# Performance work log

Measured on AMD Instinct MI355X. Metric: run time of the kernel, lower is better.

Reference implementation:

```python
import jax, jax.numpy as jnp
import numpy as np

B, S, G, E = 2048, 32768, 4096, 1024  # batch, source_size, n_groups(target_size), embeddings_size


def setup_inputs() -> dict:
    key = jax.random.key(0)
    k_x, k_w, k_we, k_perm = jax.random.split(key, 4)
    x = jax.random.normal(k_x, (B, S), dtype=jnp.float32)
    W = jax.random.normal(k_w, (E, G), dtype=jnp.float32) * 0.02  # Linear(target_size -> embed, no bias)
    # per-element weights for 'w_sum' groups (concatenated Linear(group_size,1) weights)
    w_elem = jax.random.normal(k_we, (S,), dtype=jnp.float32) * 0.1
    perm = jax.random.permutation(k_perm, S).astype(jnp.int32)
    # ragged group boundaries: n_groups groups, each size >= 1, summing to S
    rng = np.random.default_rng(0)
    cuts = np.sort(rng.choice(np.arange(1, S), G - 1, replace=False))
    sizes = np.diff(np.concatenate([[0], cuts, [S]]))
    segment_ids = jnp.asarray(np.repeat(np.arange(G), sizes), dtype=jnp.int32)
    # aggregation type per group: 0='sum', 1='or', 2='w_sum'
    agg_type = jnp.asarray(rng.integers(0, 3, G), dtype=jnp.int32)
    return {"x": x, "W": W, "w_elem": w_elem, "perm": perm,
            "segment_ids": segment_ids, "agg_type": agg_type}


def reference(x, W, w_elem, perm, segment_ids, agg_type):
    # gather via groups_permute
    xp = x[:, perm]  # [B, S]
    # fused ragged per-group reductions, segment axis first: [S, B] -> [G, B]
    xt = xp.T
    seg_sum = jax.ops.segment_sum(xt, segment_ids, num_segments=G)              # jnp.sum per group
    seg_wsum = jax.ops.segment_sum(xt * w_elem[:, None], segment_ids, num_segments=G)  # Linear(g,1) per group
    seg_nnz = jax.ops.segment_sum((xt != 0).astype(x.dtype), segment_ids, num_segments=G)
    seg_or = (seg_nnz > 0).astype(x.dtype)                                       # jnp.any per group (bool -> float on hstack)
    a = agg_type[:, None]
    y = jnp.where(a == 0, seg_sum, jnp.where(a == 1, seg_or, seg_wsum)).T        # [B, G]
    # relu + Linear(target_size -> embeddings_size, no bias)
    return jnp.einsum('bg,eg->be', jax.nn.relu(y), W)
```

## Files before the change

kernel.cpp:

```cpp
#include <hip/hip_runtime.h>
#include <hip/hip_bf16.h>

#define B_DIM 2048
#define S_DIM 32768
#define G_DIM 4096
#define E_DIM 1024
#define KSPLIT 4
#define KCHUNK (G_DIM / KSPLIT)

typedef __bf16 bf16x8 __attribute__((ext_vector_type(8)));
typedef float f32x4 __attribute__((ext_vector_type(4)));

__device__ __forceinline__ unsigned short f2bf(float f) {
  unsigned int u = __builtin_bit_cast(unsigned int, f);
  u += 0x7FFFu + ((u >> 16) & 1u);
  return (unsigned short)(u >> 16);
}

__device__ __forceinline__ void async16(void* lds, const void* g) {
  __builtin_amdgcn_global_load_lds(
      (const __attribute__((address_space(1))) unsigned int*)g,
      (__attribute__((address_space(3))) unsigned int*)lds, 16, 0, 0);
}

__device__ __forceinline__ void lds_add(float* p, float v) {
  unsigned off = (unsigned)(size_t)(__attribute__((address_space(3))) float*)p;
  asm volatile("ds_add_f32 %0, %1" :: "v"(off), "v"(v));
}

__global__ __launch_bounds__(256) void setup_meta(
    const float* __restrict__ w_elem, const int* __restrict__ perm,
    const int* __restrict__ segid, const int* __restrict__ agg,
    unsigned* __restrict__ meta1) {
  int s = blockIdx.x * 256 + threadIdx.x;
  if (s >= S_DIM) return;
  int g = segid[s];
  int a = agg[g];
  float cm = (a == 0) ? 1.0f : (a == 2 ? w_elem[s] : 0.0f);
  meta1[s] = (unsigned)perm[s] | (a == 1 ? 0x8000u : 0u) |
             ((unsigned)f2bf(cm) << 16);
}

__global__ __launch_bounds__(256) void setup_runs(
    const int* __restrict__ segid, unsigned* __restrict__ metaH,
    unsigned short* __restrict__ metaG) {
  int t = blockIdx.x * 256 + threadIdx.x;
  if (t >= S_DIM / 32) return;
  int s0 = t * 32;
  int prev = (s0 == 0) ? -1 : segid[s0 - 1];
  unsigned m = 0;
#pragma unroll
  for (int c = 0; c < 8; ++c) {
    int4 gw = *reinterpret_cast<const int4*>(segid + s0 + c * 4);
    if (gw.x != prev) m |= 1u << (c * 4 + 0);
    if (gw.y != gw.x) m |= 1u << (c * 4 + 1);
    if (gw.z != gw.y) m |= 1u << (c * 4 + 2);
    if (gw.w != gw.z) m |= 1u << (c * 4 + 3);
    prev = gw.w;
  }
  metaH[t] = m;
  metaG[t] = (unsigned short)segid[s0];
}

__global__ __launch_bounds__(256) void conv_w(const float* __restrict__ W,
                                              unsigned short* __restrict__ Wb) {
  size_t i = ((size_t)blockIdx.x * 256 + threadIdx.x) * 4;
  float4 v = *reinterpret_cast<const float4*>(W + i);
  ushort4 o;
  o.x = f2bf(v.x);
  o.y = f2bf(v.y);
  o.z = f2bf(v.z);
  o.w = f2bf(v.w);
  *reinterpret_cast<ushort4*>(Wb + i) = o;
}

__global__ __launch_bounds__(1024, 8) void seg_reduce(
    const float* __restrict__ x, const unsigned* __restrict__ meta1,
    const unsigned* __restrict__ metaH, const unsigned short* __restrict__ metaG,
    const int* __restrict__ agg, unsigned short* __restrict__ y) {
  __shared__ unsigned short xrow[S_DIM];
  __shared__ float acc[G_DIM];
  const int t = threadIdx.x;
  const int b = blockIdx.x;

#pragma unroll
  for (int i = 0; i < G_DIM / 1024; ++i) acc[t + i * 1024] = 0.0f;

  const float4* xg = reinterpret_cast<const float4*>(x + (size_t)b * S_DIM);
#pragma unroll
  for (int i = 0; i < S_DIM / 4 / 1024; ++i) {
    float4 v = xg[i * 1024 + t];
    unsigned short h0 = __builtin_bit_cast(unsigned short, (__bf16)v.x);
    unsigned short h1 = __builtin_bit_cast(unsigned short, (__bf16)v.y);
    unsigned short h2 = __builtin_bit_cast(unsigned short, (__bf16)v.z);
    unsigned short h3 = __builtin_bit_cast(unsigned short, (__bf16)v.w);
    uint2 p;
    p.x = (unsigned)h0 | ((unsigned)h1 << 16);
    p.y = (unsigned)h2 | ((unsigned)h3 << 16);
    *reinterpret_cast<uint2*>(&xrow[(i * 1024 + t) * 4]) = p;
  }
  __syncthreads();

  const int s0 = t * 32;
  const unsigned mrun = metaH[t];
  const bool firstPlain = (mrun & 1u) != 0;
  int g = metaG[t];
  float sum = 0.0f;
  int nflush = 0;

  for (int h = 0; h < 2; ++h) {
    const int sb = s0 + h * 16;
    uint4 ma = *reinterpret_cast<const uint4*>(meta1 + sb);
    uint4 mb = *reinterpret_cast<const uint4*>(meta1 + sb + 4);
    uint4 mc = *reinterpret_cast<const uint4*>(meta1 + sb + 8);
    uint4 md = *reinterpret_cast<const uint4*>(meta1 + sb + 12);
    unsigned m[16] = {ma.x, ma.y, ma.z, ma.w, mb.x, mb.y, mb.z, mb.w,
                      mc.x, mc.y, mc.z, mc.w, md.x, md.y, md.z, md.w};
    unsigned short xu[16];
#pragma unroll
    for (int j = 0; j < 16; ++j) xu[j] = xrow[m[j] & 0x7FFF];
    const unsigned mh = mrun >> (h * 16);
#pragma unroll
    for (int j = 0; j < 16; ++j) {
      if (h + j > 0 && (mh & (1u << j))) {
        if (nflush == 0 && !firstPlain) {
          lds_add(&acc[g], sum);
        } else {
          acc[g] = sum;
        }
        ++nflush;
        sum = 0.0f;
        ++g;
      }
      float xv = __builtin_bit_cast(float, (unsigned)xu[j] << 16);
      float cm = __builtin_bit_cast(float, m[j] & 0xFFFF0000u);
      float v = (m[j] & 0x8000u) ? (xu[j] ? 1.0f : 0.0f) : xv * cm;
      sum += v;
    }
  }
  lds_add(&acc[g], sum);

  asm volatile("s_waitcnt lgkmcnt(0)" ::: "memory");
  __syncthreads();

#pragma unroll
  for (int i = 0; i < G_DIM / 1024; ++i) {
    int g2 = t + i * 1024;
    float v = acc[g2];
    if (agg[g2] == 1) v = (v > 0.0f) ? 1.0f : 0.0f;
    v = fmaxf(v, 0.0f);
    y[(size_t)b * G_DIM + g2] = f2bf(v);
  }
}

__global__ __launch_bounds__(256) void gemm_bt(
    const unsigned short* __restrict__ A,
    const unsigned short* __restrict__ Bw,
    float* __restrict__ part) {
  __shared__ __align__(16) unsigned short As[64 * 64];
  __shared__ __align__(16) unsigned short Bs[64 * 64];
  const int t = threadIdx.x;
  const int lane = t & 63;
  const int wid = t >> 6;
  const int wr = wid >> 1;
  const int wc = wid & 1;
  const int row0 = blockIdx.y * 64;
  const int col0 = blockIdx.x * 64;
  const int kc = blockIdx.z;

  const int r_ = t >> 3;
  const int s_ = t & 7;
  const int ksw = (s_ ^ (r_ & 7)) * 8;
  const unsigned short* Ag0 = A + (size_t)(row0 + r_) * G_DIM + ksw;
  const unsigned short* Ag1 = A + (size_t)(row0 + r_ + 32) * G_DIM + ksw;
  const unsigned short* Bg0 = Bw + (size_t)(col0 + r_) * G_DIM + ksw;
  const unsigned short* Bg1 = Bw + (size_t)(col0 + r_ + 32) * G_DIM + ksw;

  char* AsB = (char*)As;
  char* BsB = (char*)Bs;
  char* dA0 = AsB + wid * 1024;
  char* dA1 = AsB + 4096 + wid * 1024;
  char* dB0 = BsB + wid * 1024;
  char* dB1 = BsB + 4096 + wid * 1024;

  const int lm = lane & 15;
  const int lk = lane >> 4;

  f32x4 acc[2][2] = {};

  for (int kt = kc * KCHUNK; kt < (kc + 1) * KCHUNK; kt += 64) {
    async16(dA0, Ag0 + kt);
    async16(dA1, Ag1 + kt);
    async16(dB0, Bg0 + kt);
    async16(dB1, Bg1 + kt);
    __syncthreads();
#pragma unroll
    for (int kk = 0; kk < 2; ++kk) {
      bf16x8 af[2], bfr[2];
#pragma unroll
      for (int m = 0; m < 2; ++m) {
        int row = wr * 32 + m * 16 + lm;
        int slot = (kk * 4 + lk) ^ (row & 7);
        af[m] = *(const bf16x8*)(AsB + row * 128 + slot * 16);
      }
#pragma unroll
      for (int n = 0; n < 2; ++n) {
        int row = wc * 32 + n * 16 + lm;
        int slot = (kk * 4 + lk) ^ (row & 7);
        bfr[n] = *(const bf16x8*)(BsB + row * 128 + slot * 16);
      }
#pragma unroll
      for (int m = 0; m < 2; ++m)
#pragma unroll
        for (int n = 0; n < 2; ++n)
          acc[m][n] = __builtin_amdgcn_mfma_f32_16x16x32_bf16(af[m], bfr[n],
                                                              acc[m][n], 0, 0, 0);
    }
    __syncthreads();
  }

  float* P = part + (size_t)kc * B_DIM * E_DIM;
#pragma unroll
  for (int m = 0; m < 2; ++m) {
    int r = row0 + wr * 32 + m * 16 + lk * 4;
#pragma unroll
    for (int n = 0; n < 2; ++n) {
      int c = col0 + wc * 32 + n * 16 + lm;
#pragma unroll
      for (int q = 0; q < 4; ++q) {
        P[(size_t)(r + q) * E_DIM + c] = acc[m][n][q];
      }
    }
  }
}

__global__ __launch_bounds__(256) void reduce_part(
    const float* __restrict__ part, float* __restrict__ C) {
  const size_t i = ((size_t)blockIdx.x * 256 + threadIdx.x) * 4;
  const size_t n = (size_t)B_DIM * E_DIM;
  float4 v0 = *reinterpret_cast<const float4*>(part + i);
  float4 v1 = *reinterpret_cast<const float4*>(part + n + i);
  float4 v2 = *reinterpret_cast<const float4*>(part + 2 * n + i);
  float4 v3 = *reinterpret_cast<const float4*>(part + 3 * n + i);
  float4 o;
  o.x = (v0.x + v1.x) + (v2.x + v3.x);
  o.y = (v0.y + v1.y) + (v2.y + v3.y);
  o.z = (v0.z + v1.z) + (v2.z + v3.z);
  o.w = (v0.w + v1.w) + (v2.w + v3.w);
  *reinterpret_cast<float4*>(C + i) = o;
}

extern "C" void kernel_launch(void* const* d_in, const int* in_sizes, int n_in,
                              void* d_out, int out_size, void* d_ws, size_t ws_size,
                              hipStream_t stream) {
  const float* x = (const float*)d_in[0];
  const float* W = (const float*)d_in[1];
  const float* w_elem = (const float*)d_in[2];
  const int* perm = (const int*)d_in[3];
  const int* segid = (const int*)d_in[4];
  const int* agg = (const int*)d_in[5];
  float* out = (float*)d_out;

  char* ws = (char*)d_ws;
  unsigned short* y = (unsigned short*)ws;
  unsigned short* Wb =
      (unsigned short*)(ws + (size_t)B_DIM * G_DIM * 2);
  float* part = (float*)(ws + (size_t)B_DIM * G_DIM * 2 +
                         (size_t)E_DIM * G_DIM * 2);
  unsigned* meta1 = (unsigned*)((char*)part +
                                (size_t)KSPLIT * B_DIM * E_DIM * 4);
  unsigned* metaH = (unsigned*)((char*)meta1 + (size_t)S_DIM * 4);
  unsigned short* metaG = (unsigned short*)((char*)metaH + (S_DIM / 32) * 4);

  hipLaunchKernelGGL(setup_meta, dim3(S_DIM / 256), dim3(256), 0, stream,
                     w_elem, perm, segid, agg, meta1);
  hipLaunchKernelGGL(setup_runs, dim3((S_DIM / 32) / 256), dim3(256), 0,
                     stream, segid, metaH, metaG);
  hipLaunchKernelGGL(conv_w, dim3((E_DIM * G_DIM / 4) / 256), dim3(256), 0,
                     stream, W, Wb);
  hipLaunchKernelGGL(seg_reduce, dim3(B_DIM), dim3(1024), 0, stream, x, meta1,
                     metaH, metaG, agg, y);
  hipLaunchKernelGGL(gemm_bt, dim3(E_DIM / 64, B_DIM / 64, KSPLIT), dim3(256),
                     0, stream, y, Wb, part);
  hipLaunchKernelGGL(reduce_part,
                     dim3(((size_t)B_DIM * E_DIM / 4) / 256), dim3(256), 0,
                     stream, part, out);
}
```

Before: 130.0 us.

## Store split-K partials in bf16 and replace LDS atomics with scan-style segment merge

The split-K GEMM now writes its partial sums as bf16 rather than fp32, which halves the traffic to write and re-read the partial buffer. The reduce kernel is changed to match, handling 8 elements per thread. In seg_reduce, the ds_add_f32 atomics for segments that cross thread boundaries are removed. Each thread now stores its leading partial in scratch LDS that reuses xrow, and the thread that starts a segment walks forward summing the following threads' partials. This adds two barriers and a serial walk whose length depends on how many threads a segment spans, and rounding partials to bf16 adds precision loss.

```diff
diff --git a/kernel.cpp b/kernel.cpp
--- a/kernel.cpp
+++ b/kernel.cpp
@@ -17,15 +17,17 @@
   return (unsigned short)(u >> 16);
 }
 
+__device__ __forceinline__ float bfl(unsigned u) {
+  return __builtin_bit_cast(float, u << 16);
+}
+__device__ __forceinline__ float bfh(unsigned u) {
+  return __builtin_bit_cast(float, u & 0xFFFF0000u);
+}
+
 __device__ __forceinline__ void async16(void* lds, const void* g) {
   __builtin_amdgcn_global_load_lds(
       (const __attribute__((address_space(1))) unsigned int*)g,
       (__attribute__((address_space(3))) unsigned int*)lds, 16, 0, 0);
-}
-
-__device__ __forceinline__ void lds_add(float* p, float v) {
-  unsigned off = (unsigned)(size_t)(__attribute__((address_space(3))) float*)p;
-  asm volatile("ds_add_f32 %0, %1" :: "v"(off), "v"(v));
 }
 
 __global__ __launch_bounds__(256) void setup_meta(
@@ -78,13 +80,19 @@
     const float* __restrict__ x, const unsigned* __restrict__ meta1,
     const unsigned* __restrict__ metaH, const unsigned short* __restrict__ metaG,
     const int* __restrict__ agg, unsigned short* __restrict__ y) {
-  __shared__ unsigned short xrow[S_DIM];
+  __shared__ __align__(16) unsigned short xrow[S_DIM];
   __shared__ float acc[G_DIM];
+  float* scr = reinterpret_cast<float*>(xrow);
   const int t = threadIdx.x;
   const int b = blockIdx.x;
 
 #pragma unroll
   for (int i = 0; i < G_DIM / 1024; ++i) acc[t + i * 1024] = 0.0f;
+
+  const unsigned mrun = metaH[t];
+  const unsigned nextH = (t < 1023) ? metaH[t + 1] : 1u;
+  const bool fp = (mrun & 1u) != 0;
+  int g = metaG[t];
 
   const float4* xg = reinterpret_cast<const float4*>(x + (size_t)b * S_DIM);
 #pragma unroll
@@ -102,11 +110,8 @@
   __syncthreads();
 
   const int s0 = t * 32;
-  const unsigned mrun = metaH[t];
-  const bool firstPlain = (mrun & 1u) != 0;
-  int g = metaG[t];
-  float sum = 0.0f;
-  int nflush = 0;
+  float sum = 0.0f, lead = 0.0f;
+  int nf = 0;
 
   for (int h = 0; h < 2; ++h) {
     const int sb = s0 + h * 16;
@@ -123,24 +128,39 @@
 #pragma unroll
     for (int j = 0; j < 16; ++j) {
       if (h + j > 0 && (mh & (1u << j))) {
-        if (nflush == 0 && !firstPlain) {
-          lds_add(&acc[g], sum);
+        if (nf == 0 && !fp) {
+          lead = sum;
         } else {
           acc[g] = sum;
         }
-        ++nflush;
+        ++nf;
         sum = 0.0f;
         ++g;
       }
-      float xv = __builtin_bit_cast(float, (unsigned)xu[j] << 16);
-      float cm = __builtin_bit_cast(float, m[j] & 0xFFFF0000u);
+      float xv = bfl((unsigned)xu[j]);
+      float cm = bfh(m[j]);
       float v = (m[j] & 0x8000u) ? (xu[j] ? 1.0f : 0.0f) : xv * cm;
       sum += v;
     }
   }
-  lds_add(&acc[g], sum);
-
-  asm volatile("s_waitcnt lgkmcnt(0)" ::: "memory");
+
+  __syncthreads();
+
+  scr[t] = fp ? 0.0f : (nf == 0 ? sum : lead);
+  __syncthreads();
+
+  if (mrun != 0) {
+    float tot = sum;
+    unsigned fh = nextH;
+    int k = t + 1;
+    while (k < 1024) {
+      tot += scr[k];
+      if (fh) break;
+      ++k;
+      fh = metaH[k];
+    }
+    acc[g] = tot;
+  }
   __syncthreads();
 
 #pragma unroll
@@ -156,7 +176,7 @@
 __global__ __launch_bounds__(256) void gemm_bt(
     const unsigned short* __restrict__ A,
     const unsigned short* __restrict__ Bw,
-    float* __restrict__ part) {
+    unsigned short* __restrict__ part) {
   __shared__ __align__(16) unsigned short As[64 * 64];
   __shared__ __align__(16) unsigned short Bs[64 * 64];
   const int t = threadIdx.x;
@@ -219,7 +239,7 @@
     __syncthreads();
   }
 
-  float* P = part + (size_t)kc * B_DIM * E_DIM;
+  unsigned short* P = part + (size_t)kc * B_DIM * E_DIM;
 #pragma unroll
   for (int m = 0; m < 2; ++m) {
     int r = row0 + wr * 32 + m * 16 + lk * 4;
@@ -228,26 +248,31 @@
       int c = col0 + wc * 32 + n * 16 + lm;
 #pragma unroll
       for (int q = 0; q < 4; ++q) {
-        P[(size_t)(r + q) * E_DIM + c] = acc[m][n][q];
+        P[(size_t)(r + q) * E_DIM + c] = f2bf(acc[m][n][q]);
       }
     }
   }
 }
 
 __global__ __launch_bounds__(256) void reduce_part(
-    const float* __restrict__ part, float* __restrict__ C) {
-  const size_t i = ((size_t)blockIdx.x * 256 + threadIdx.x) * 4;
+    const unsigned short* __restrict__ part, float* __restrict__ C) {
+  const size_t i = ((size_t)blockIdx.x * 256 + threadIdx.x) * 8;
   const size_t n = (size_t)B_DIM * E_DIM;
-  float4 v0 = *reinterpret_cast<const float4*>(part + i);
-  float4 v1 = *reinterpret_cast<const float4*>(part + n + i);
-  float4 v2 = *reinterpret_cast<const float4*>(part + 2 * n + i);
-  float4 v3 = *reinterpret_cast<const float4*>(part + 3 * n + i);
-  float4 o;
-  o.x = (v0.x + v1.x) + (v2.x + v3.x);
-  o.y = (v0.y + v1.y) + (v2.y + v3.y);
-  o.z = (v0.z + v1.z) + (v2.z + v3.z);
-  o.w = (v0.w + v1.w) + (v2.w + v3.w);
-  *reinterpret_cast<float4*>(C + i) = o;
+  float e[8] = {};
+#pragma unroll
+  for (int p = 0; p < KSPLIT; ++p) {
+    uint4 v = *reinterpret_cast<const uint4*>(part + p * n + i);
+    unsigned w[4] = {v.x, v.y, v.z, v.w};
+#pragma unroll
+    for (int q = 0; q < 4; ++q) {
+      e[2 * q] += bfl(w[q]);
+      e[2 * q + 1] += bfh(w[q]);
+    }
+  }
+  float4 o0 = {e[0], e[1], e[2], e[3]};
+  float4 o1 = {e[4], e[5], e[6], e[7]};
+  *reinterpret_cast<float4*>(C + i) = o0;
+  *reinterpret_cast<float4*>(C + i + 4) = o1;
 }
 
 extern "C" void kernel_launch(void* const* d_in, const int* in_sizes, int n_in,
@@ -265,10 +290,11 @@
   unsigned short* y = (unsigned short*)ws;
   unsigned short* Wb =
       (unsigned short*)(ws + (size_t)B_DIM * G_DIM * 2);
-  float* part = (float*)(ws + (size_t)B_DIM * G_DIM * 2 +
-                         (size_t)E_DIM * G_DIM * 2);
-  unsigned* meta1 = (unsigned*)((char*)part +
-                                (size_t)KSPLIT * B_DIM * E_DIM * 4);
+  unsigned short* part =
+      (unsigned short*)(ws + (size_t)B_DIM * G_DIM * 2 +
+                        (size_t)E_DIM * G_DIM * 2);
+  unsigned* meta1 =
+      (unsigned*)((char*)part + (size_t)KSPLIT * B_DIM * E_DIM * 2);
   unsigned* metaH = (unsigned*)((char*)meta1 + (size_t)S_DIM * 4);
   unsigned short* metaG = (unsigned short*)((char*)metaH + (S_DIM / 32) * 4);
 
@@ -283,6 +309,6 @@
   hipLaunchKernelGGL(gemm_bt, dim3(E_DIM / 64, B_DIM / 64, KSPLIT), dim3(256),
                      0, stream, y, Wb, part);
   hipLaunchKernelGGL(reduce_part,
-                     dim3(((size_t)B_DIM * E_DIM / 4) / 256), dim3(256), 0,
+                     dim3(((size_t)B_DIM * E_DIM / 8) / 256), dim3(256), 0,
                      stream, part, out);
 }
```

Result: faster. 126.0 us (-3.1%).
